# Performance work log

Hardware: AMD Instinct MI355X
Metric: run time of the kernel (lower is better)

Reference implementation:

```python
import jax, jax.numpy as jnp
import numpy as np
import math

EPS = 1e-5
GROUPS = 32

def group_norm(x, gamma, beta, groups=GROUPS, eps=EPS):
    B, C, H, W = x.shape
    xr = x.reshape(B, groups, C // groups, H, W)
    m = xr.mean(axis=(2, 3, 4), keepdims=True)
    v = xr.var(axis=(2, 3, 4), keepdims=True)
    xr = (xr - m) * jax.lax.rsqrt(v + eps)
    x = xr.reshape(B, C, H, W)
    return x * gamma[None, :, None, None] + beta[None, :, None, None]

def swish(x):
    return x * jax.nn.sigmoid(x)

def conv2d(x, w, b=None, padding='SAME'):
    # x: NCHW, w: OIHW
    y = jax.lax.conv_general_dilated(x, w, window_strides=(1, 1), padding=padding,
                                     dimension_numbers=('NCHW', 'OIHW', 'NCHW'))
    if b is not None:
        y = y + b[None, :, None, None]
    return y

def setup_inputs() -> dict:
    key = jax.random.key(0)
    ks = jax.random.split(key, 24)
    B, C, H, W = 16, 256, 32, 32
    NE = 256  # noise_level_emb_dim
    s = 0.02
    inp = {
        'x': jax.random.normal(ks[0], (B, C, H, W), jnp.float32),
        'time_emb': jax.random.normal(ks[1], (B, NE), jnp.float32),
        'c': jax.random.normal(ks[2], (B, C, H, W), jnp.float32),
        # block1: GroupNorm + Swish + Conv3x3(dim -> dim_out)
        'gn1_g': jnp.ones((C,), jnp.float32),
        'gn1_b': jnp.zeros((C,), jnp.float32),
        'conv1_w': jax.random.normal(ks[3], (C, C, 3, 3), jnp.float32) * s,
        'conv1_b': jnp.zeros((C,), jnp.float32),
        # FeatureWiseAffine linear (use_affine_level=False): Linear(NE -> dim_out)
        'noise_w': jax.random.normal(ks[4], (C, NE), jnp.float32) * s,
        'noise_b': jnp.zeros((C,), jnp.float32),
        # block2: GroupNorm + Swish + Conv3x3(dim_out -> dim_out)
        'gn2_g': jnp.ones((C,), jnp.float32),
        'gn2_b': jnp.zeros((C,), jnp.float32),
        'conv2_w': jax.random.normal(ks[5], (C, C, 3, 3), jnp.float32) * s,
        'conv2_b': jnp.zeros((C,), jnp.float32),
        # c_func: Conv1x1(dim_out -> dim_out)
        'cfunc_w': jax.random.normal(ks[6], (C, C, 1, 1), jnp.float32) * s,
        'cfunc_b': jnp.zeros((C,), jnp.float32),
        # attention: GroupNorm, qkv Conv1x1 (no bias), out Conv1x1
        'attn_gn_g': jnp.ones((C,), jnp.float32),
        'attn_gn_b': jnp.zeros((C,), jnp.float32),
        'qkv_w': jax.random.normal(ks[7], (3 * C, C, 1, 1), jnp.float32) * s,
        'out_w': jax.random.normal(ks[8], (C, C, 1, 1), jnp.float32) * s,
        'out_b': jnp.zeros((C,), jnp.float32),
    }
    return inp

def reference(x, time_emb, c,
              gn1_g, gn1_b, conv1_w, conv1_b,
              noise_w, noise_b,
              gn2_g, gn2_b, conv2_w, conv2_b,
              cfunc_w, cfunc_b,
              attn_gn_g, attn_gn_b, qkv_w, out_w, out_b):
    B, C, H, W = x.shape
    # ---- ResnetBlock ----
    h = conv2d(swish(group_norm(x, gn1_g, gn1_b)), conv1_w, conv1_b)
    # FeatureWiseAffine (additive): h + Linear(time_emb) broadcast over HxW
    h = h + (time_emb @ noise_w.T + noise_b)[:, :, None, None]
    h = conv2d(swish(group_norm(h, gn2_g, gn2_b)), conv2_w, conv2_b)
    h = conv2d(c, cfunc_w, cfunc_b) + h
    h = h + x  # res_conv is Identity since dim == dim_out
    # ---- SelfAttention (n_head=1) ----
    n = group_norm(h, attn_gn_g, attn_gn_b)
    qkv = conv2d(n, qkv_w)                       # [B, 3C, H, W]
    q, k, v = jnp.split(qkv.reshape(B, 3 * C, H * W), 3, axis=1)  # each [B, C, HW]
    scores = jnp.einsum('bcs,bct->bst', q, k) / math.sqrt(C)      # [B, HW, HW]
    attn = jax.nn.softmax(scores, axis=-1)
    o = jnp.einsum('bst,bct->bcs', attn, v).reshape(B, C, H, W)
    o = conv2d(o, out_w, out_b)
    return o + h
```

## Files before the change

kernel.cpp:

```cpp
#include <hip/hip_runtime.h>
#include <hip/hip_bf16.h>
#include <math.h>

typedef __hip_bfloat16 bf16;
typedef short short8 __attribute__((ext_vector_type(8)));
typedef float floatx4 __attribute__((ext_vector_type(4)));

#define NB 16
#define NC 256
#define NHW 1024
#define NNE 256
#define NP (NB*NC*NHW)

__device__ __forceinline__ unsigned short f2bu(float f){
  bf16 h = (bf16)f; return *(unsigned short*)&h;
}

__device__ __forceinline__ void gload_lds16(const short* g, short* l){
  __builtin_amdgcn_global_load_lds(
      (const __attribute__((address_space(1))) void*)g,
      (__attribute__((address_space(3))) void*)l, 16, 0, 0);
}

__global__ __launch_bounds__(256)
void prep_mega_kernel(const float* __restrict__ w1, const float* __restrict__ w2,
                      short* __restrict__ wp1, short* __restrict__ wp2,
                      float* __restrict__ st,
                      const float* __restrict__ wq, const float* __restrict__ wc,
                      const float* __restrict__ wo,
                      short* __restrict__ wqp, short* __restrict__ wcp,
                      short* __restrict__ wop,
                      const float* __restrict__ c_in, short* __restrict__ cp,
                      const float* __restrict__ emb, const float* __restrict__ nw,
                      const float* __restrict__ nb, float* __restrict__ na,
                      const float* __restrict__ x, const float* __restrict__ gn1_g,
                      const float* __restrict__ gn1_b, short* __restrict__ xp){
  __shared__ float smem[8224];
  const int blk = blockIdx.x, tid = threadIdx.x;

  if (blk < 512){
    int co = blk & 255;
    const float* w = (blk < 256) ? w1 : w2;
    short* wp = (blk < 256) ? wp1 : wp2;
    if (blk == 0){
      for (int i=tid;i<4096;i+=256) st[i] = 0.f;
    }
    float* tmp = smem;
    for (int i=tid;i<2304;i+=256) tmp[i] = w[(size_t)co*2304 + i];
    __syncthreads();
    for (int j=tid;j<2304;j+=256){
      int tap = j>>8, ci = j&255;
      wp[(((size_t)tap*8 + (ci>>5))*NC + co)*32 + (ci&31)] = (short)f2bu(tmp[ci*9 + tap]);
    }
  } else if (blk < 1792){
    int bq = blk - 512;
    if (bq < 768){
      float v = wq[(size_t)bq*256 + tid];
      wqp[(((size_t)(tid>>5))*768 + bq)*32 + (tid&31)] = (short)f2bu(v);
    } else if (bq < 1024){
      int co = bq - 768;
      float v = wc[(size_t)co*256 + tid];
      wcp[(((size_t)(tid>>5))*256 + co)*32 + (tid&31)] = (short)f2bu(v);
    } else {
      int co = bq - 1024;
      float v = wo[(size_t)co*256 + tid];
      wop[(((size_t)(tid>>5))*256 + co)*32 + (tid&31)] = (short)f2bu(v);
    }
  } else if (blk < 2304){
    int j = blk - 1792;
    int pxc = j&3, cc = (j>>2)&7, b = j>>5;
    float* ld = smem;
    size_t gbase = ((size_t)b*NC + cc*32)*NHW + pxc*256;
    for (int r=0;r<32;r++) ld[r*257 + tid] = c_in[gbase + (size_t)r*NHW + tid];
    __syncthreads();
    short* dst = cp + (((size_t)b*8 + cc)*NHW + pxc*256)*32;
    for (int it=0;it<4;it++){
      int pxl = it*64 + (tid>>2), ckl = tid&3;
      short8 pk;
      #pragma unroll
      for (int e=0;e<8;e++) pk[e] = (short)f2bu(ld[(ckl*8+e)*257 + pxl]);
      *(short8*)(dst + (size_t)pxl*32 + ckl*8) = pk;
    }
  } else if (blk < 2320){
    int b = blk - 2304, c = tid;
    float* e = smem;
    e[c] = emb[b*NNE + c];
    __syncthreads();
    float acc = nb[c];
    for (int k=0;k<NNE;k++) acc += e[k]*nw[c*NNE+k];
    na[b*NC + c] = acc;
  } else {
    int j = blk - 2320;
    int b = j >> 5, g = j & 31;
    const int GSZ = 8*NHW;
    size_t base = ((size_t)b*NC + g*8)*NHW;
    float s = 0.f, ss = 0.f;
    for (int i = tid; i < GSZ; i += 256){
      float v = x[base+i];
      s += v; ss += v*v;
    }
    float* rs = smem; float* rq = smem + 256;
    rs[tid] = s; rq[tid] = ss;
    __syncthreads();
    for (int off=128; off>0; off>>=1){
      if (tid < off){ rs[tid]+=rs[tid+off]; rq[tid]+=rq[tid+off]; }
      __syncthreads();
    }
    float mean = rs[0] * (1.f/GSZ);
    float var  = rq[0] * (1.f/GSZ) - mean*mean;
    float inv  = rsqrtf(var + 1e-5f);
    float gm[8], bt[8];
    #pragma unroll
    for (int jj=0;jj<8;jj++){ gm[jj] = gn1_g[g*8+jj]*inv; bt[jj] = gn1_b[g*8+jj]; }
    short* dst = xp + (((size_t)b*8 + (g>>2))*NHW)*32 + (g&3)*8;
    for (int px = tid; px < NHW; px += 256){
      short8 pk;
      #pragma unroll
      for (int jj=0;jj<8;jj++){
        float v = (x[base + jj*NHW + px] - mean)*gm[jj] + bt[jj];
        v = v / (1.f + __expf(-v));
        pk[jj] = (short)f2bu(v);
      }
      *(short8*)(dst + (size_t)px*32) = pk;
    }
  }
}

template<bool SWISH>
__global__ void gn_post_kernel(const float* __restrict__ src, const float* __restrict__ st,
                               const float* __restrict__ gamma, const float* __restrict__ beta,
                               short* __restrict__ xp){
  int b = blockIdx.x >> 5, g = blockIdx.x & 31;
  size_t base = ((size_t)b*NC + g*8)*NHW;
  int tid = threadIdx.x;
  float s  = st[(b*32+g)*2+0];
  float ss = st[(b*32+g)*2+1];
  float mean = s * (1.f/8192.f);
  float var  = ss * (1.f/8192.f) - mean*mean;
  float inv  = rsqrtf(var + 1e-5f);
  float gm[8], bt[8];
  #pragma unroll
  for (int j=0;j<8;j++){ gm[j] = gamma[g*8+j]*inv; bt[j] = beta[g*8+j]; }
  short* dst = xp + (((size_t)b*8 + (g>>2))*NHW)*32 + (g&3)*8;
  for (int px = tid; px < NHW; px += 256){
    short8 pk;
    #pragma unroll
    for (int j=0;j<8;j++){
      float v = (src[base + j*NHW + px] - mean)*gm[j] + bt[j];
      if (SWISH) v = v / (1.f + __expf(-v));
      pk[j] = (short)f2bu(v);
    }
    *(short8*)(dst + (size_t)px*32) = pk;
  }
}

__global__ __launch_bounds__(256,2)
void conv3_mfma_kernel(const short* __restrict__ xp, const short* __restrict__ wp,
                       const float* __restrict__ bias, const float* __restrict__ bias_bc,
                       const float* __restrict__ addf, float* __restrict__ out,
                       float* __restrict__ st, const short* __restrict__ zpad){
  const int b = blockIdx.z, bx = blockIdx.x, by = blockIdx.y;
  const int tid = threadIdx.x, wave = tid>>6, lane = tid&63;
  const int quad = lane>>4, lm = lane&15;
  const int co0 = by*64;
  const int px0 = bx*128, yb = bx*4;

  __shared__ short Sb0[12288], Sb1[12288], Sb2[12288];

  const int rowt = tid>>3;
  const int g2   = (tid&7) ^ ((tid>>3)&7);
  const int kq2  = g2 & 3;
  const int ccs2 = g2 >> 2;
  const size_t b8 = (size_t)b*8*NHW*32;

  auto STAGE = [&](int j, short* S){
    const int tap = j>>2, ccp = j&3;
    const int dyp = (tap*11)>>5;
    const int dx  = tap - dyp*3 - 1;
    const int dy  = dyp - 1;
    const short* wsrc = wp + (size_t)(tap*8 + ccp*2 + ccs2)*8192 + (co0 + rowt)*32 + kq2*8;
    #pragma unroll
    for (int i=0;i<2;i++)
      gload_lds16(wsrc + i*(32*32), S + tid*8 + i*2048);
    const short* xstep = xp + b8 + (size_t)(ccp*2 + ccs2)*(NHW*32);
    const int xx = rowt + dx;
    const bool xok = (unsigned)xx < 32u;
    #pragma unroll
    for (int i=0;i<4;i++){
      const int y = yb + i + dy;
      const short* src = (xok && (unsigned)y < 32u)
                       ? (xstep + (y*32 + xx)*32 + kq2*8)
                       : (zpad + kq2*8);
      gload_lds16(src, S + 4096 + tid*8 + i*2048);
    }
  };

  floatx4 acc[4][2];
  #pragma unroll
  for (int mt=0;mt<4;mt++)
    #pragma unroll
    for (int nt=0;nt<2;nt++) acc[mt][nt] = (floatx4){0.f,0.f,0.f,0.f};

  const int sl = lm & 7;
  auto STEP = [&](int j, short* S){
    asm volatile("s_waitcnt vmcnt(12)" ::: "memory");
    __builtin_amdgcn_s_barrier();
    __builtin_amdgcn_sched_barrier(0);
    short8 Af[2][4], Bf[2][2];
    #pragma unroll
    for (int ka=0;ka<2;ka++){
      const int slot = ((ka*4 + quad) ^ sl) << 3;
      #pragma unroll
      for (int mt=0;mt<4;mt++)
        Af[ka][mt] = *(const short8*)(S + (mt*16+lm)*64 + slot);
      #pragma unroll
      for (int nt=0;nt<2;nt++)
        Bf[ka][nt] = *(const short8*)(S + 4096 + (wave*32 + nt*16 + lm)*64 + slot);
    }
    asm volatile("s_waitcnt lgkmcnt(0)" ::: "memory");
    __builtin_amdgcn_sched_barrier(0);
    __builtin_amdgcn_s_barrier();
    int jn = j + 3; if (jn > 35) jn = 35;
    STAGE(jn, S);
    __builtin_amdgcn_s_setprio(1);
    #pragma unroll
    for (int ka=0;ka<2;ka++)
      #pragma unroll
      for (int mt=0;mt<4;mt++)
        #pragma unroll
        for (int nt=0;nt<2;nt++)
          acc[mt][nt] = __builtin_amdgcn_mfma_f32_16x16x32_bf16(Af[ka][mt], Bf[ka][nt], acc[mt][nt], 0,0,0);
    __builtin_amdgcn_s_setprio(0);
  };

  STAGE(0, Sb0); STAGE(1, Sb1); STAGE(2, Sb2);
  for (int jt=0; jt<36; jt+=3){
    STEP(jt+0, Sb0);
    STEP(jt+1, Sb1);
    STEP(jt+2, Sb2);
  }

  float gs[4], gq[4];
  #pragma unroll
  for (int mt=0;mt<4;mt++){ gs[mt]=0.f; gq[mt]=0.f; }
  #pragma unroll
  for (int mt=0;mt<4;mt++){
    #pragma unroll
    for (int r=0;r<4;r++){
      int co = co0 + mt*16 + quad*4 + r;
      float bb = bias[co] + (bias_bc ? bias_bc[b*NC + co] : 0.f);
      size_t ob = ((size_t)b*NC + co)*NHW + px0 + wave*32;
      #pragma unroll
      for (int nt=0;nt<2;nt++){
        size_t oi = ob + nt*16 + lm;
        float v = acc[mt][nt][r] + bb;
        if (addf) v += addf[oi];
        out[oi] = v;
        gs[mt] += v; gq[mt] += v*v;
      }
    }
  }
  #pragma unroll
  for (int mt=0;mt<4;mt++){
    float s = gs[mt], q = gq[mt];
    #pragma unroll
    for (int o=1;o<32;o<<=1){ s += __shfl_xor(s, o, 64); q += __shfl_xor(q, o, 64); }
    if ((lane&31) == 0){
      int g = (co0>>3) + mt*2 + (quad>>1);
      atomicAdd(&st[(b*32+g)*2+0], s);
      atomicAdd(&st[(b*32+g)*2+1], q);
    }
  }
}

__global__ __launch_bounds__(256)
void gemm_cfunc_kernel(const short* __restrict__ cp, const short* __restrict__ wcp,
                       const float* __restrict__ bias, const float* __restrict__ xres,
                       float* __restrict__ out){
  const int b = blockIdx.z;
  const int tid = threadIdx.x, wave = tid>>6, lane = tid&63;
  const int quad = lane>>4, lm = lane&15;
  const int M0 = blockIdx.y*128 + (wave>>1)*64;
  const int N0 = blockIdx.x*128 + (wave&1)*64;
  floatx4 acc[4][4];
  #pragma unroll
  for (int mt=0;mt<4;mt++)
    #pragma unroll
    for (int nt=0;nt<4;nt++) acc[mt][nt] = (floatx4){0.f,0.f,0.f,0.f};
  #pragma unroll
  for (int kk=0;kk<8;kk++){
    short8 af[4], bfr[4];
    #pragma unroll
    for (int mt=0;mt<4;mt++)
      af[mt] = *(const short8*)(wcp + ((size_t)kk*256 + M0 + mt*16 + lm)*32 + quad*8);
    #pragma unroll
    for (int nt=0;nt<4;nt++)
      bfr[nt] = *(const short8*)(cp + (((size_t)b*8 + kk)*NHW + N0 + nt*16 + lm)*32 + quad*8);
    #pragma unroll
    for (int mt=0;mt<4;mt++)
      #pragma unroll
      for (int nt=0;nt<4;nt++)
        acc[mt][nt] = __builtin_amdgcn_mfma_f32_16x16x32_bf16(af[mt], bfr[nt], acc[mt][nt], 0,0,0);
  }
  #pragma unroll
  for (int mt=0;mt<4;mt++){
    #pragma unroll
    for (int r=0;r<4;r++){
      int co = M0 + mt*16 + quad*4 + r;
      float bb = bias[co];
      size_t ob = ((size_t)b*NC + co)*NHW + N0;
      #pragma unroll
      for (int nt=0;nt<4;nt++){
        size_t oi = ob + nt*16 + lm;
        out[oi] = acc[mt][nt][r] + bb + xres[oi];
      }
    }
  }
}

__global__ __launch_bounds__(256)
void gemm_qkv_kernel(const short* __restrict__ ntp, const short* __restrict__ wqp,
                     short* __restrict__ qp, short* __restrict__ kp, short* __restrict__ vp){
  const int b = blockIdx.z;
  const int tid = threadIdx.x, wave = tid>>6, lane = tid&63;
  const int quad = lane>>4, lm = lane&15;
  const int M0 = blockIdx.y*128 + (wave>>1)*64;
  const int N0 = blockIdx.x*128 + (wave&1)*64;
  floatx4 acc[4][4];
  #pragma unroll
  for (int mt=0;mt<4;mt++)
    #pragma unroll
    for (int nt=0;nt<4;nt++) acc[mt][nt] = (floatx4){0.f,0.f,0.f,0.f};
  #pragma unroll
  for (int kk=0;kk<8;kk++){
    short8 af[4], bfr[4];
    #pragma unroll
    for (int mt=0;mt<4;mt++)
      af[mt] = *(const short8*)(wqp + ((size_t)kk*768 + M0 + mt*16 + lm)*32 + quad*8);
    #pragma unroll
    for (int nt=0;nt<4;nt++)
      bfr[nt] = *(const short8*)(ntp + (((size_t)b*8 + kk)*NHW + N0 + nt*16 + lm)*32 + quad*8);
    #pragma unroll
    for (int mt=0;mt<4;mt++)
      #pragma unroll
      for (int nt=0;nt<4;nt++)
        acc[mt][nt] = __builtin_amdgcn_mfma_f32_16x16x32_bf16(af[mt], bfr[nt], acc[mt][nt], 0,0,0);
  }
  #pragma unroll
  for (int mt=0;mt<4;mt++){
    int co_base = M0 + mt*16 + quad*4;
    int sec = co_base >> 8;
    int c = co_base & 255;
    #pragma unroll
    for (int nt=0;nt<4;nt++){
      int s = N0 + nt*16 + lm;
      if (sec < 2){
        unsigned short t0 = f2bu(acc[mt][nt][0]), t1 = f2bu(acc[mt][nt][1]);
        unsigned short t2 = f2bu(acc[mt][nt][2]), t3 = f2bu(acc[mt][nt][3]);
        uint2 w2; w2.x = ((unsigned)t1<<16)|t0; w2.y = ((unsigned)t3<<16)|t2;
        short* dst = (sec==0) ? qp : kp;
        *(uint2*)(dst + (((size_t)b*8 + (c>>5))*NHW + s)*32 + (c&31)) = w2;
      } else {
        #pragma unroll
        for (int r=0;r<4;r++)
          vp[(((size_t)b*32 + (s>>5))*NC + c + r)*32 + (s&31)] = (short)f2bu(acc[mt][nt][r]);
      }
    }
  }
}

__global__ __launch_bounds__(1024)
void attn_mfma_kernel(const short* __restrict__ qp, const short* __restrict__ kp,
                      const short* __restrict__ vp, short* __restrict__ op){
  const int bx = blockIdx.x;
  const int b = bx & 15;
  const int s0 = (bx >> 4) * 64;
  const int tid = threadIdx.x, wave = tid>>6, lane = tid&63;
  const int quad = lane>>4, lm = lane&15;

  __shared__ short P[64*1024];
  __shared__ float red[64][16];
  __shared__ float fred[64];

  floatx4 sc[4][4];
  #pragma unroll
  for (int rt=0;rt<4;rt++)
    #pragma unroll
    for (int ti=0;ti<4;ti++) sc[rt][ti] = (floatx4){0.f,0.f,0.f,0.f};

  const int colb = wave*64;
  #pragma unroll
  for (int h=0;h<8;h++){
    const size_t hb = ((size_t)b*8 + h)*NHW;
    short8 aq[4], kf[4];
    #pragma unroll
    for (int rt=0;rt<4;rt++)
      aq[rt] = *(const short8*)(qp + (hb + s0 + rt*16 + lm)*32 + quad*8);
    #pragma unroll
    for (int ti=0;ti<4;ti++)
      kf[ti] = *(const short8*)(kp + (hb + colb + ti*16 + lm)*32 + quad*8);
    #pragma unroll
    for (int rt=0;rt<4;rt++)
      #pragma unroll
      for (int ti=0;ti<4;ti++)
        sc[rt][ti] = __builtin_amdgcn_mfma_f32_16x16x32_bf16(aq[rt], kf[ti], sc[rt][ti], 0,0,0);
  }

  const float scale = 0.0625f;
  float mx[4][4];
  #pragma unroll
  for (int rt=0;rt<4;rt++)
    #pragma unroll
    for (int r=0;r<4;r++) mx[rt][r] = -1e30f;
  #pragma unroll
  for (int rt=0;rt<4;rt++)
    #pragma unroll
    for (int ti=0;ti<4;ti++)
      #pragma unroll
      for (int r=0;r<4;r++){
        float v = sc[rt][ti][r]*scale;
        sc[rt][ti][r] = v;
        mx[rt][r] = fmaxf(mx[rt][r], v);
      }
  #pragma unroll
  for (int o=1;o<16;o<<=1)
    #pragma unroll
    for (int rt=0;rt<4;rt++)
      #pragma unroll
      for (int r=0;r<4;r++) mx[rt][r] = fmaxf(mx[rt][r], __shfl_xor(mx[rt][r], o, 64));
  if (lm==0){
    #pragma unroll
    for (int rt=0;rt<4;rt++)
      #pragma unroll
      for (int r=0;r<4;r++) red[rt*16 + quad*4 + r][wave] = mx[rt][r];
  }
  __syncthreads();
  {
    float v = red[tid>>4][tid&15];
    #pragma unroll
    for (int o=1;o<16;o<<=1) v = fmaxf(v, __shfl_xor(v, o, 64));
    if ((tid&15)==0) fred[tid>>4] = v;
  }
  __syncthreads();
  float fmr[4][4], sm[4][4];
  #pragma unroll
  for (int rt=0;rt<4;rt++)
    #pragma unroll
    for (int r=0;r<4;r++){ fmr[rt][r] = fred[rt*16 + quad*4 + r]; sm[rt][r] = 0.f; }
  #pragma unroll
  for (int rt=0;rt<4;rt++)
    #pragma unroll
    for (int ti=0;ti<4;ti++)
      #pragma unroll
      for (int r=0;r<4;r++){
        float e = __expf(sc[rt][ti][r] - fmr[rt][r]);
        sc[rt][ti][r] = e;
        sm[rt][r] += e;
      }
  #pragma unroll
  for (int o=1;o<16;o<<=1)
    #pragma unroll
    for (int rt=0;rt<4;rt++)
      #pragma unroll
      for (int r=0;r<4;r++) sm[rt][r] += __shfl_xor(sm[rt][r], o, 64);
  __syncthreads();
  if (lm==0){
    #pragma unroll
    for (int rt=0;rt<4;rt++)
      #pragma unroll
      for (int r=0;r<4;r++) red[rt*16 + quad*4 + r][wave] = sm[rt][r];
  }
  __syncthreads();
  {
    float v = red[tid>>4][tid&15];
    #pragma unroll
    for (int o=1;o<16;o<<=1) v += __shfl_xor(v, o, 64);
    if ((tid&15)==0) fred[tid>>4] = 1.f/v;
  }
  __syncthreads();
  float fir[4][4];
  #pragma unroll
  for (int rt=0;rt<4;rt++)
    #pragma unroll
    for (int r=0;r<4;r++) fir[rt][r] = fred[rt*16 + quad*4 + r];
  #pragma unroll
  for (int rt=0;rt<4;rt++)
    #pragma unroll
    for (int ti=0;ti<4;ti++)
      #pragma unroll
      for (int r=0;r<4;r++){
        int row = rt*16 + quad*4 + r;
        int col = colb + ti*16 + lm;
        int off = row*1024 + ((((col>>3) ^ (row&7))&127)<<3) + (col&7);
        P[off] = (short)f2bu(sc[rt][ti][r]*fir[rt][r]);
      }
  __syncthreads();

  const int cg = wave>>1, sh = wave&1;
  const int ch0 = cg*32;
  floatx4 oacc[2][2];
  #pragma unroll
  for (int mt=0;mt<2;mt++)
    #pragma unroll
    for (int nt=0;nt<2;nt++) oacc[mt][nt] = (floatx4){0.f,0.f,0.f,0.f};

  #pragma unroll
  for (int kk=0;kk<32;kk++){
    short8 pf[2], vf[2];
    #pragma unroll
    for (int mt=0;mt<2;mt++){
      int row = sh*32 + mt*16 + lm;
      int off = row*1024 + ((((kk*4 + quad) ^ (row&7))&127)<<3);
      pf[mt] = *(const short8*)(&P[off]);
    }
    #pragma unroll
    for (int nt=0;nt<2;nt++)
      vf[nt] = *(const short8*)(vp + (((size_t)b*32 + kk)*NC + ch0 + nt*16 + lm)*32 + quad*8);
    #pragma unroll
    for (int mt=0;mt<2;mt++)
      #pragma unroll
      for (int nt=0;nt<2;nt++)
        oacc[mt][nt] = __builtin_amdgcn_mfma_f32_16x16x32_bf16(pf[mt], vf[nt], oacc[mt][nt], 0,0,0);
  }

  #pragma unroll
  for (int nt=0;nt<2;nt++){
    int c = ch0 + nt*16 + lm;
    int cc = c>>5, cl = c&31;
    #pragma unroll
    for (int mt=0;mt<2;mt++)
      #pragma unroll
      for (int r=0;r<4;r++){
        int s = s0 + sh*32 + mt*16 + quad*4 + r;
        op[(((size_t)b*8 + cc)*NHW + s)*32 + cl] = (short)f2bu(oacc[mt][nt][r]);
      }
  }
}

__global__ __launch_bounds__(256)
void outproj_mfma_kernel(const short* __restrict__ op, const short* __restrict__ wop,
                         const float* __restrict__ obias, const float* __restrict__ h,
                         float* __restrict__ out){
  const int b = blockIdx.z;
  const int tid = threadIdx.x, wave = tid>>6, lane = tid&63;
  const int quad = lane>>4, lm = lane&15;
  const int M0 = blockIdx.y*128 + (wave>>1)*64;
  const int N0 = blockIdx.x*128 + (wave&1)*64;
  floatx4 acc[4][4];
  #pragma unroll
  for (int mt=0;mt<4;mt++)
    #pragma unroll
    for (int nt=0;nt<4;nt++) acc[mt][nt] = (floatx4){0.f,0.f,0.f,0.f};
  #pragma unroll
  for (int kk=0;kk<8;kk++){
    short8 af[4], bfr[4];
    #pragma unroll
    for (int mt=0;mt<4;mt++)
      af[mt] = *(const short8*)(wop + ((size_t)kk*256 + M0 + mt*16 + lm)*32 + quad*8);
    #pragma unroll
    for (int nt=0;nt<4;nt++)
      bfr[nt] = *(const short8*)(op + (((size_t)b*8 + kk)*NHW + N0 + nt*16 + lm)*32 + quad*8);
    #pragma unroll
    for (int mt=0;mt<4;mt++)
      #pragma unroll
      for (int nt=0;nt<4;nt++)
        acc[mt][nt] = __builtin_amdgcn_mfma_f32_16x16x32_bf16(af[mt], bfr[nt], acc[mt][nt], 0,0,0);
  }
  #pragma unroll
  for (int mt=0;mt<4;mt++){
    #pragma unroll
    for (int r=0;r<4;r++){
      int co = M0 + mt*16 + quad*4 + r;
      float bb = obias[co];
      size_t ob = ((size_t)b*NC + co)*NHW + N0;
      #pragma unroll
      for (int nt=0;nt<4;nt++){
        size_t oi = ob + nt*16 + lm;
        out[oi] = acc[mt][nt][r] + bb + h[oi];
      }
    }
  }
}

extern "C" void kernel_launch(void* const* d_in, const int* in_sizes, int n_in,
                              void* d_out, int out_size, void* d_ws, size_t ws_size,
                              hipStream_t stream){
  const float* x        = (const float*)d_in[0];
  const float* time_emb = (const float*)d_in[1];
  const float* c_in     = (const float*)d_in[2];
  const float* gn1_g    = (const float*)d_in[3];
  const float* gn1_b    = (const float*)d_in[4];
  const float* conv1_w  = (const float*)d_in[5];
  const float* conv1_b  = (const float*)d_in[6];
  const float* noise_w  = (const float*)d_in[7];
  const float* noise_b  = (const float*)d_in[8];
  const float* gn2_g    = (const float*)d_in[9];
  const float* gn2_b    = (const float*)d_in[10];
  const float* conv2_w  = (const float*)d_in[11];
  const float* conv2_b  = (const float*)d_in[12];
  const float* cfunc_w  = (const float*)d_in[13];
  const float* cfunc_b  = (const float*)d_in[14];
  const float* agn_g    = (const float*)d_in[15];
  const float* agn_b    = (const float*)d_in[16];
  const float* qkv_w    = (const float*)d_in[17];
  const float* out_w    = (const float*)d_in[18];
  const float* out_b    = (const float*)d_in[19];
  float* outp = (float*)d_out;

  float* ws = (float*)d_ws;
  float* buf_h = ws;
  float* buf_t = buf_h + NP;
  short* xpb   = (short*)(buf_t + NP);
  short* qp    = xpb + NP;
  short* kp    = qp + NP;
  short* vp    = kp + NP;
  short* wp1   = vp + NP;
  short* wp2   = wp1 + 589824;
  short* wqp   = wp2 + 589824;
  short* wcp   = wqp + 196608;
  short* wop   = wcp + 65536;
  float* na    = (float*)(wop + 65536);
  float* st    = na + NB*NC;
  float* st2   = st;
  float* st3   = st + 1024;
  const short* zpadp = (const short*)(st + 2048);
  short* cp    = (short*)buf_t;
  short* op    = (short*)buf_t;

  prep_mega_kernel<<<2832, 256, 0, stream>>>(
      conv1_w, conv2_w, wp1, wp2, st,
      qkv_w, cfunc_w, out_w, wqp, wcp, wop,
      c_in, cp,
      time_emb, noise_w, noise_b, na,
      x, gn1_g, gn1_b, xpb);
  conv3_mfma_kernel<<<dim3(8, 4, NB), 256, 0, stream>>>(xpb, wp1, conv1_b, na, nullptr, buf_h, st2, zpadp);
  gn_post_kernel<true><<<NB*32, 256, 0, stream>>>(buf_h, st2, gn2_g, gn2_b, xpb);
  gemm_cfunc_kernel<<<dim3(8,2,NB), 256, 0, stream>>>(cp, wcp, cfunc_b, x, buf_h);
  conv3_mfma_kernel<<<dim3(8, 4, NB), 256, 0, stream>>>(xpb, wp2, conv2_b, nullptr, buf_h, buf_h, st3, zpadp);
  gn_post_kernel<false><<<NB*32, 256, 0, stream>>>(buf_h, st3, agn_g, agn_b, xpb);
  gemm_qkv_kernel<<<dim3(8,6,NB), 256, 0, stream>>>(xpb, wqp, qp, kp, vp);
  attn_mfma_kernel<<<256, 1024, 0, stream>>>(qp, kp, vp, op);
  outproj_mfma_kernel<<<dim3(8,2,NB), 256, 0, stream>>>(op, wop, out_b, buf_h, outp);
}
```

Baseline: 334.1 us.

## Fuse 1x1 c_func GEMM into second conv3x3 as extra K steps

```diff
diff --git a/kernel.cpp b/kernel.cpp
--- a/kernel.cpp
+++ b/kernel.cpp
@@ -154,11 +154,14 @@
   }
 }
 
+template<int NSTEP>
 __global__ __launch_bounds__(256,2)
 void conv3_mfma_kernel(const short* __restrict__ xp, const short* __restrict__ wp,
                        const float* __restrict__ bias, const float* __restrict__ bias_bc,
                        const float* __restrict__ addf, float* __restrict__ out,
-                       float* __restrict__ st, const short* __restrict__ zpad){
+                       float* __restrict__ st, const short* __restrict__ zpad,
+                       const short* __restrict__ cp2, const short* __restrict__ wcp2,
+                       const float* __restrict__ bias2){
   const int b = blockIdx.z, bx = blockIdx.x, by = blockIdx.y;
   const int tid = threadIdx.x, wave = tid>>6, lane = tid&63;
   const int quad = lane>>4, lm = lane&15;
@@ -174,6 +177,20 @@
   const size_t b8 = (size_t)b*8*NHW*32;
 
   auto STAGE = [&](int j, short* S){
+    if constexpr (NSTEP > 36){
+      if (j >= 36){
+        const int cc = j - 36;
+        const short* wsrc = wcp2 + (size_t)(cc*2 + ccs2)*8192 + (co0 + rowt)*32 + kq2*8;
+        #pragma unroll
+        for (int i=0;i<2;i++)
+          gload_lds16(wsrc + i*(32*32), S + tid*8 + i*2048);
+        const short* xstep = cp2 + b8 + (size_t)(cc*2 + ccs2)*(NHW*32);
+        #pragma unroll
+        for (int i=0;i<4;i++)
+          gload_lds16(xstep + ((yb+i)*32 + rowt)*32 + kq2*8, S + 4096 + tid*8 + i*2048);
+        return;
+      }
+    }
     const int tap = j>>2, ccp = j&3;
     const int dyp = (tap*11)>>5;
     const int dx  = tap - dyp*3 - 1;
@@ -220,7 +237,7 @@
     asm volatile("s_waitcnt lgkmcnt(0)" ::: "memory");
     __builtin_amdgcn_sched_barrier(0);
     __builtin_amdgcn_s_barrier();
-    int jn = j + 3; if (jn > 35) jn = 35;
+    int jn = j + 3; if (jn > NSTEP-1) jn = NSTEP-1;
     STAGE(jn, S);
     __builtin_amdgcn_s_setprio(1);
     #pragma unroll
@@ -239,6 +256,12 @@
     STEP(jt+1, Sb1);
     STEP(jt+2, Sb2);
   }
+  if constexpr (NSTEP == 40){
+    STEP(36, Sb0);
+    STEP(37, Sb1);
+    STEP(38, Sb2);
+    STEP(39, Sb0);
+  }
 
   float gs[4], gq[4];
   #pragma unroll
@@ -248,7 +271,7 @@
     #pragma unroll
     for (int r=0;r<4;r++){
       int co = co0 + mt*16 + quad*4 + r;
-      float bb = bias[co] + (bias_bc ? bias_bc[b*NC + co] : 0.f);
+      float bb = bias[co] + (bias2 ? bias2[co] : 0.f) + (bias_bc ? bias_bc[b*NC + co] : 0.f);
       size_t ob = ((size_t)b*NC + co)*NHW + px0 + wave*32;
       #pragma unroll
       for (int nt=0;nt<2;nt++){
@@ -269,51 +292,6 @@
       int g = (co0>>3) + mt*2 + (quad>>1);
       atomicAdd(&st[(b*32+g)*2+0], s);
       atomicAdd(&st[(b*32+g)*2+1], q);
-    }
-  }
-}
-
-__global__ __launch_bounds__(256)
-void gemm_cfunc_kernel(const short* __restrict__ cp, const short* __restrict__ wcp,
-                       const float* __restrict__ bias, const float* __restrict__ xres,
-                       float* __restrict__ out){
-  const int b = blockIdx.z;
-  const int tid = threadIdx.x, wave = tid>>6, lane = tid&63;
-  const int quad = lane>>4, lm = lane&15;
-  const int M0 = blockIdx.y*128 + (wave>>1)*64;
-  const int N0 = blockIdx.x*128 + (wave&1)*64;
-  floatx4 acc[4][4];
-  #pragma unroll
-  for (int mt=0;mt<4;mt++)
-    #pragma unroll
-    for (int nt=0;nt<4;nt++) acc[mt][nt] = (floatx4){0.f,0.f,0.f,0.f};
-  #pragma unroll
-  for (int kk=0;kk<8;kk++){
-    short8 af[4], bfr[4];
-    #pragma unroll
-    for (int mt=0;mt<4;mt++)
-      af[mt] = *(const short8*)(wcp + ((size_t)kk*256 + M0 + mt*16 + lm)*32 + quad*8);
-    #pragma unroll
-    for (int nt=0;nt<4;nt++)
-      bfr[nt] = *(const short8*)(cp + (((size_t)b*8 + kk)*NHW + N0 + nt*16 + lm)*32 + quad*8);
-    #pragma unroll
-    for (int mt=0;mt<4;mt++)
-      #pragma unroll
-      for (int nt=0;nt<4;nt++)
-        acc[mt][nt] = __builtin_amdgcn_mfma_f32_16x16x32_bf16(af[mt], bfr[nt], acc[mt][nt], 0,0,0);
-  }
-  #pragma unroll
-  for (int mt=0;mt<4;mt++){
-    #pragma unroll
-    for (int r=0;r<4;r++){
-      int co = M0 + mt*16 + quad*4 + r;
-      float bb = bias[co];
-      size_t ob = ((size_t)b*NC + co)*NHW + N0;
-      #pragma unroll
-      for (int nt=0;nt<4;nt++){
-        size_t oi = ob + nt*16 + lm;
-        out[oi] = acc[mt][nt][r] + bb + xres[oi];
-      }
     }
   }
 }
@@ -633,10 +611,11 @@
       c_in, cp,
       time_emb, noise_w, noise_b, na,
       x, gn1_g, gn1_b, xpb);
-  conv3_mfma_kernel<<<dim3(8, 4, NB), 256, 0, stream>>>(xpb, wp1, conv1_b, na, nullptr, buf_h, st2, zpadp);
+  conv3_mfma_kernel<36><<<dim3(8, 4, NB), 256, 0, stream>>>(
+      xpb, wp1, conv1_b, na, nullptr, buf_h, st2, zpadp, nullptr, nullptr, nullptr);
   gn_post_kernel<true><<<NB*32, 256, 0, stream>>>(buf_h, st2, gn2_g, gn2_b, xpb);
-  gemm_cfunc_kernel<<<dim3(8,2,NB), 256, 0, stream>>>(cp, wcp, cfunc_b, x, buf_h);
-  conv3_mfma_kernel<<<dim3(8, 4, NB), 256, 0, stream>>>(xpb, wp2, conv2_b, nullptr, buf_h, buf_h, st3, zpadp);
+  conv3_mfma_kernel<40><<<dim3(8, 4, NB), 256, 0, stream>>>(
+      xpb, wp2, conv2_b, nullptr, x, buf_h, st3, zpadp, cp, wcp, cfunc_b);
   gn_post_kernel<false><<<NB*32, 256, 0, stream>>>(buf_h, st3, agn_g, agn_b, xpb);
   gemm_qkv_kernel<<<dim3(8,6,NB), 256, 0, stream>>>(xpb, wqp, qp, kp, vp);
   attn_mfma_kernel<<<256, 1024, 0, stream>>>(qp, kp, vp, op);
```

Measured after the change: 317.4 us. 1.05x faster.
